# Performance work log

Measured on AMD Instinct MI355X. Metric: run time of the kernel, lower is better.

The kernel has to match this reference:

```python
import jax, jax.numpy as jnp
import numpy as np

N_NODES = 50000
N_HEDGES = 10000
N_MEMB = 800000
IN_SIZE = 256
HEADS = 4
OUT_SIZE = 64


def setup_inputs() -> dict:
    key = jax.random.key(0)
    k1, k2, k3, k4, k5 = jax.random.split(key, 5)
    x = jax.random.normal(k1, (N_NODES, IN_SIZE), dtype=jnp.float32)
    # Linear weight stored as [in, out*heads] so projection is x @ W (same math as torch Linear)
    W = jax.random.normal(k2, (IN_SIZE, OUT_SIZE * HEADS), dtype=jnp.float32) * (1.0 / np.sqrt(IN_SIZE))
    att_e = jax.random.normal(k3, (1, HEADS, OUT_SIZE), dtype=jnp.float32) * 0.1
    node_idx = jax.random.randint(k4, (N_MEMB,), 0, N_NODES, dtype=jnp.int64)
    hedge_idx = jax.random.randint(k5, (N_MEMB,), 0, N_HEDGES, dtype=jnp.int64)
    return {"x": x, "W": W, "att_e": att_e, "node_idx": node_idx,
            "hedge_idx": hedge_idx, "num_hyperedges": N_HEDGES}


def reference(x, W, att_e, node_idx, hedge_idx, num_hyperedges):
    # Dropout is treated as eval-mode identity.
    N = x.shape[0]
    H, D = att_e.shape[1], att_e.shape[2]
    xp = (x @ W).reshape(N, H, D)                                   # [N,H,D]
    # Stage 1: mean-aggregate node features into hyperedges (belongs-to)
    ones = jnp.ones(node_idx.shape[0], dtype=x.dtype)
    deg = jax.ops.segment_sum(ones, hedge_idx, num_segments=num_hyperedges)  # [E]
    he = jax.ops.segment_sum(xp[node_idx], hedge_idx, num_segments=num_hyperedges)
    he = he / jnp.maximum(deg, 1.0)[:, None, None]                  # [E,H,D]
    # Attention logit per hyperedge
    alpha_e = jax.nn.leaky_relu(jnp.sum(he * att_e, axis=-1), 0.2)  # [E,H]
    # Stage 2: edge_softmax over 'contains' edges grouped by destination node
    ae = alpha_e[hedge_idx]                                         # [M,H]
    mx = jax.ops.segment_max(ae, node_idx, num_segments=N)          # [N,H]
    ex = jnp.exp(ae - mx[node_idx])
    den = jax.ops.segment_sum(ex, node_idx, num_segments=N)         # [N,H]
    a = ex / den[node_idx]                                          # [M,H]
    # Attention-weighted scatter-sum of hyperedge features to nodes
    out = jax.ops.segment_sum(he[hedge_idx] * a[:, :, None], node_idx, num_segments=N)  # [N,H,D]
    return out.reshape(N, H * D)
```

## Files before the change

kernel.cpp:

```cpp
#include <hip/hip_runtime.h>
#include <hip/hip_fp16.h>
#include <math.h>

#define N_NODES  50000
#define N_HEDGES 10000
#define N_MEMB   800000
#define KIN      256
#define CH       256
#define HEADS    4
#define HCAP     160
#define NCAP     48
#define GR       16

#define NCHUNK      125
#define CHUNK4      1600
#define XCVT_F4     3200000
#define XCVT_BLOCKS 1563
#define WCVT_BLOCKS 8
#define HED_W       2500
#define NOD_W       12500

typedef _Float16 half2v __attribute__((ext_vector_type(2)));

__device__ inline float2 h2f(unsigned u) {
    __half2 h = __builtin_bit_cast(__half2, u);
    return __half22float2(h);
}
__device__ inline unsigned f2h(float a, float b) {
    return __builtin_bit_cast(unsigned, __floats2half2_rn(a, b));
}
__device__ inline float4 u2tof4(uint2 u) {
    float2 lo = h2f(u.x), hi = h2f(u.y);
    return make_float4(lo.x, lo.y, hi.x, hi.y);
}
__device__ inline void acc4(float4& a, float4 f) {
    a.x += f.x; a.y += f.y; a.z += f.z; a.w += f.w;
}
__device__ inline void fmaU4(float4& A, float4& B, float w, uint4 g) {
    float2 f0 = h2f(g.x), f1 = h2f(g.y), f2 = h2f(g.z), f3 = h2f(g.w);
    A.x += w * f0.x; A.y += w * f0.y; A.z += w * f1.x; A.w += w * f1.y;
    B.x += w * f2.x; B.y += w * f2.y; B.z += w * f3.x; B.w += w * f3.y;
}

__global__ __launch_bounds__(1024)
void k_hist_cvt(const int4* __restrict__ ni4, const int4* __restrict__ hi4,
                unsigned char* __restrict__ htab, unsigned char* __restrict__ ntab,
                const float4* __restrict__ x4, uint2* __restrict__ x16,
                const float* __restrict__ Wf, unsigned* __restrict__ Wp) {
    __shared__ unsigned sh[HED_W + NOD_W];
    int bid = blockIdx.x, tid = threadIdx.x;
    if (bid < NCHUNK) {
        int chunk = bid;
        for (int i = tid; i < HED_W + NOD_W; i += 1024) sh[i] = 0;
        __syncthreads();
        int base4 = chunk * CHUNK4;
        for (int i = tid; i < CHUNK4; i += 1024) {
            int4 e = hi4[base4 + i]; int4 n = ni4[base4 + i];
            #pragma unroll
            for (int k = 0; k < 4; k++) {
                int ev = (&e.x)[k], nv = (&n.x)[k];
                atomicAdd(&sh[ev >> 2], 1u << ((ev & 3) * 8));
                atomicAdd(&sh[HED_W + (nv >> 2)], 1u << ((nv & 3) * 8));
            }
        }
        __syncthreads();
        unsigned* hd = (unsigned*)(htab + (size_t)chunk * N_HEDGES);
        for (int i = tid; i < HED_W; i += 1024) hd[i] = sh[i];
        unsigned* nd = (unsigned*)(ntab + (size_t)chunk * N_NODES);
        for (int i = tid; i < NOD_W; i += 1024) nd[i] = sh[HED_W + i];
    } else if (bid < NCHUNK + XCVT_BLOCKS) {
        int i0 = (bid - NCHUNK) * 2048 + tid;
        #pragma unroll
        for (int r = 0; r < 2; r++) {
            int idx = i0 + r * 1024;
            if (idx < XCVT_F4) {
                float4 v = x4[idx];
                uint2 u; u.x = f2h(v.x, v.y); u.y = f2h(v.z, v.w);
                x16[idx] = u;
            }
        }
    } else {
        int tg = (bid - NCHUNK - XCVT_BLOCKS) * 1024 + tid;
        #pragma unroll
        for (int r = 0; r < 4; r++) {
            int wI = tg + r * 8192;
            int k2 = wI >> 8, c = wI & 255;
            Wp[wI] = f2h(Wf[(size_t)(2 * k2) * CH + c], Wf[(size_t)(2 * k2 + 1) * CH + c]);
        }
    }
}

__global__ __launch_bounds__(1024)
void k_scan(unsigned char* __restrict__ htab, unsigned char* __restrict__ ntab,
            int* __restrict__ hdeg, int* __restrict__ ndeg) {
    int b = blockIdx.x * 1024 + threadIdx.x;
    if (b < N_HEDGES) {
        int run = 0;
        for (int c = 0; c < NCHUNK; c++) {
            size_t idx = (size_t)c * N_HEDGES + b;
            int v = htab[idx];
            htab[idx] = (unsigned char)run;
            run += v;
        }
        hdeg[b] = run;
    } else if (b < N_HEDGES + N_NODES) {
        int nb = b - N_HEDGES;
        int run = 0;
        for (int c = 0; c < NCHUNK; c++) {
            size_t idx = (size_t)c * N_NODES + nb;
            int v = ntab[idx];
            ntab[idx] = (unsigned char)run;
            run += v;
        }
        ndeg[nb] = run;
    }
}

__global__ __launch_bounds__(1024)
void k_place(const int4* __restrict__ ni4, const int4* __restrict__ hi4,
             const unsigned char* __restrict__ htab, const unsigned char* __restrict__ ntab,
             int* __restrict__ hmem, int* __restrict__ nhedge) {
    __shared__ unsigned sh[HED_W + NOD_W];
    int bid = blockIdx.x, tid = threadIdx.x;
    int chunk = bid;
    for (int i = tid; i < HED_W + NOD_W; i += 1024) sh[i] = 0;
    __syncthreads();
    int base4 = chunk * CHUNK4;
    const unsigned char* hoff = htab + (size_t)chunk * N_HEDGES;
    const unsigned char* noff = ntab + (size_t)chunk * N_NODES;
    for (int i = tid; i < CHUNK4; i += 1024) {
        int4 e = hi4[base4 + i]; int4 n = ni4[base4 + i];
        #pragma unroll
        for (int k = 0; k < 4; k++) {
            int ev = (&e.x)[k], nv = (&n.x)[k];
            unsigned oldh = atomicAdd(&sh[ev >> 2], 1u << ((ev & 3) * 8));
            int rh = (int)((oldh >> ((ev & 3) * 8)) & 0xffu);
            int posh = (int)hoff[ev] + rh;
            if (posh < HCAP) hmem[(size_t)ev * HCAP + posh] = nv;
            unsigned oldn = atomicAdd(&sh[HED_W + (nv >> 2)], 1u << ((nv & 3) * 8));
            int rn = (int)((oldn >> ((nv & 3) * 8)) & 0xffu);
            int posn = (int)noff[nv] + rn;
            if (posn < NCAP) nhedge[(size_t)nv * NCAP + posn] = ev;
        }
    }
}

__global__ __launch_bounds__(256, 8)
void k_stage1(const int* __restrict__ hdeg, const int* __restrict__ hmem,
              const uint2* __restrict__ x16, uint2* __restrict__ hx) {
    __shared__ int sidx[4][HCAP];
    int tid = threadIdx.x;
    int w = tid >> 6, lt = tid & 63;
    int e = blockIdx.x * 4 + w;
    int deg = hdeg[e];
    int degC = min(deg, HCAP);
    const int* ml = hmem + (size_t)e * HCAP;
    for (int j = lt; j < degC; j += 64) sidx[w][j] = ml[j];
    __syncthreads();
    float4 ac0 = {0,0,0,0}, ac1 = {0,0,0,0}, ac2 = {0,0,0,0}, ac3 = {0,0,0,0};
    for (int j = 0; j < degC; j += 8) {
        uint2 g[8];
        #pragma unroll
        for (int i = 0; i < 8; i++) {
            int jj = j + i; jj = jj < degC ? jj : degC - 1;
            g[i] = x16[(size_t)sidx[w][jj] * 64 + lt];
        }
        if (j + 0 < degC) acc4(ac0, u2tof4(g[0]));
        if (j + 1 < degC) acc4(ac1, u2tof4(g[1]));
        if (j + 2 < degC) acc4(ac2, u2tof4(g[2]));
        if (j + 3 < degC) acc4(ac3, u2tof4(g[3]));
        if (j + 4 < degC) acc4(ac0, u2tof4(g[4]));
        if (j + 5 < degC) acc4(ac1, u2tof4(g[5]));
        if (j + 6 < degC) acc4(ac2, u2tof4(g[6]));
        if (j + 7 < degC) acc4(ac3, u2tof4(g[7]));
    }
    float sx = (ac0.x + ac1.x) + (ac2.x + ac3.x);
    float sy = (ac0.y + ac1.y) + (ac2.y + ac3.y);
    float sz = (ac0.z + ac1.z) + (ac2.z + ac3.z);
    float sw = (ac0.w + ac1.w) + (ac2.w + ac3.w);
    float inv = deg > 0 ? 1.0f / (float)deg : 0.0f;
    uint2 o; o.x = f2h(sx * inv, sy * inv); o.y = f2h(sz * inv, sw * inv);
    hx[(size_t)e * 64 + lt] = o;
}

__global__ void k_gemm_alpha(const uint2* __restrict__ hx, const unsigned* __restrict__ Wp,
                             const float* __restrict__ att, __half* __restrict__ he,
                             float* __restrict__ alpha) {
    __shared__ unsigned xsp[GR][KIN / 2];
    int tid = threadIdx.x;
    int e0 = blockIdx.x * GR;
    #pragma unroll
    for (int jj = 0; jj < GR * 64 / 256; jj++) {
        int f = jj * 256 + tid;
        int r = f >> 6, k4 = f & 63;
        uint2 u = hx[(size_t)(e0 + r) * 64 + k4];
        xsp[r][k4 * 2] = u.x; xsp[r][k4 * 2 + 1] = u.y;
    }
    __syncthreads();
    float acc[GR];
    #pragma unroll
    for (int r = 0; r < GR; r++) acc[r] = 0.f;
    int c = tid;
    for (int k2 = 0; k2 < KIN / 2; k2++) {
        half2v wv = __builtin_bit_cast(half2v, Wp[k2 * CH + c]);
        #pragma unroll
        for (int r = 0; r < GR; r++) {
            half2v av = __builtin_bit_cast(half2v, xsp[r][k2]);
#if __has_builtin(__builtin_amdgcn_fdot2)
            acc[r] = __builtin_amdgcn_fdot2(av, wv, acc[r], false);
#else
            acc[r] += (float)av.x * (float)wv.x + (float)av.y * (float)wv.y;
#endif
        }
    }
    #pragma unroll
    for (int r = 0; r < GR; r++)
        he[(size_t)(e0 + r) * CH + c] = __float2half_rn(acc[r]);
    float av = att[c];
    int lane = tid & 63, h = tid >> 6;
    #pragma unroll
    for (int r = 0; r < GR; r++) {
        float p = acc[r] * av;
        #pragma unroll
        for (int d = 32; d >= 1; d >>= 1) p += __shfl_xor(p, d, 64);
        if (lane == 0) alpha[(e0 + r) * HEADS + h] = p > 0.f ? p : 0.2f * p;
    }
}

__global__ __launch_bounds__(256, 8)
void k_stage2(const uint4* __restrict__ heu4, const float4* __restrict__ alpha4,
              const int* __restrict__ ndeg, const int* __restrict__ nhedge,
              float4* __restrict__ out) {
    __shared__ int   nh[4][NCAP];
    __shared__ float wl[4][4][NCAP];
    int tid = threadIdx.x;
    int w = tid >> 6, L = tid & 63;
    int half = L >> 5, q = L & 31;
    int n = blockIdx.x * 4 + w;
    int deg = min(ndeg[n], NCAP);
    const int* nl = nhedge + (size_t)n * NCAP;
    if (L < deg) nh[w][L] = nl[L];
    __syncthreads();
    float4 mx = make_float4(-INFINITY, -INFINITY, -INFINITY, -INFINITY);
    float4 w4 = make_float4(0.f, 0.f, 0.f, 0.f);
    float4 aj = mx;
    if (L < deg) { aj = alpha4[nh[w][L]]; mx = aj; }
    #pragma unroll
    for (int d = 32; d >= 1; d >>= 1) {
        mx.x = fmaxf(mx.x, __shfl_xor(mx.x, d, 64));
        mx.y = fmaxf(mx.y, __shfl_xor(mx.y, d, 64));
        mx.z = fmaxf(mx.z, __shfl_xor(mx.z, d, 64));
        mx.w = fmaxf(mx.w, __shfl_xor(mx.w, d, 64));
    }
    if (L < deg) {
        w4.x = __expf(aj.x - mx.x); w4.y = __expf(aj.y - mx.y);
        w4.z = __expf(aj.z - mx.z); w4.w = __expf(aj.w - mx.w);
        wl[w][0][L] = w4.x; wl[w][1][L] = w4.y;
        wl[w][2][L] = w4.z; wl[w][3][L] = w4.w;
    }
    float4 dn = w4;
    #pragma unroll
    for (int d = 32; d >= 1; d >>= 1) {
        dn.x += __shfl_xor(dn.x, d, 64);
        dn.y += __shfl_xor(dn.y, d, 64);
        dn.z += __shfl_xor(dn.z, d, 64);
        dn.w += __shfl_xor(dn.w, d, 64);
    }
    __syncthreads();
    int h = q >> 3;
    float den = h < 2 ? (h == 0 ? dn.x : dn.y) : (h == 2 ? dn.z : dn.w);
    float4 A = make_float4(0.f, 0.f, 0.f, 0.f);
    float4 B = make_float4(0.f, 0.f, 0.f, 0.f);
    if (deg > 0) {
        for (int j = 0; j < deg; j += 8) {
            uint4 g[4]; float wgt[4];
            #pragma unroll
            for (int i = 0; i < 4; i++) {
                int jj = j + 2 * i + half;
                int jc = jj < deg ? jj : deg - 1;
                wgt[i] = jj < deg ? wl[w][h][jc] : 0.f;
                g[i] = heu4[(size_t)nh[w][jc] * 32 + q];
            }
            #pragma unroll
            for (int i = 0; i < 4; i++) fmaU4(A, B, wgt[i], g[i]);
        }
    }
    A.x += __shfl_xor(A.x, 32, 64); A.y += __shfl_xor(A.y, 32, 64);
    A.z += __shfl_xor(A.z, 32, 64); A.w += __shfl_xor(A.w, 32, 64);
    B.x += __shfl_xor(B.x, 32, 64); B.y += __shfl_xor(B.y, 32, 64);
    B.z += __shfl_xor(B.z, 32, 64); B.w += __shfl_xor(B.w, 32, 64);
    if (half == 0) {
        if (deg > 0) {
            float inv = 1.0f / den;
            A.x *= inv; A.y *= inv; A.z *= inv; A.w *= inv;
            B.x *= inv; B.y *= inv; B.z *= inv; B.w *= inv;
        }
        out[(size_t)n * 64 + 2 * q]     = A;
        out[(size_t)n * 64 + 2 * q + 1] = B;
    }
}

extern "C" void kernel_launch(void* const* d_in, const int* in_sizes, int n_in,
                              void* d_out, int out_size, void* d_ws, size_t ws_size,
                              hipStream_t stream) {
    const float* x        = (const float*)d_in[0];
    const float* W        = (const float*)d_in[1];
    const float* att      = (const float*)d_in[2];
    const int*   node_idx = (const int*)d_in[3];
    const int*   hedge_idx= (const int*)d_in[4];
    float4* out4 = (float4*)d_out;

    char* ws = (char*)d_ws;
    size_t o = 0;
    auto alloc = [&](size_t b) { size_t r = o; o += (b + 255) & ~(size_t)255; return r; };
    uint2* hx    = (uint2*)(ws + alloc(sizeof(__half) * (size_t)N_HEDGES * KIN));
    float* alpha = (float*)(ws + alloc(sizeof(float) * (size_t)N_HEDGES * HEADS));
    unsigned* Wp = (unsigned*)(ws + alloc(sizeof(unsigned) * (KIN / 2) * CH));
    int*   hdeg  = (int*)(ws + alloc(sizeof(int) * N_HEDGES));
    int*   ndeg  = (int*)(ws + alloc(sizeof(int) * N_NODES));
    size_t hmem_off = alloc(sizeof(int) * (size_t)N_HEDGES * HCAP);
    int*    hmem = (int*)(ws + hmem_off);
    __half* he   = (__half*)(ws + hmem_off);
    int*   nhedge = (int*)(ws + alloc(sizeof(int) * (size_t)N_NODES * NCAP));
    unsigned char* htab = (unsigned char*)(ws + alloc((size_t)NCHUNK * N_HEDGES));
    unsigned char* ntab = (unsigned char*)(ws + alloc((size_t)NCHUNK * N_NODES));
    if (o > ws_size) return;
    uint2* x16 = (uint2*)d_out;

    k_hist_cvt<<<NCHUNK + XCVT_BLOCKS + WCVT_BLOCKS, 1024, 0, stream>>>(
        (const int4*)node_idx, (const int4*)hedge_idx, htab, ntab,
        (const float4*)x, x16, W, Wp);
    k_scan<<<(N_HEDGES + N_NODES + 1023) / 1024, 1024, 0, stream>>>(htab, ntab, hdeg, ndeg);
    k_place<<<NCHUNK, 1024, 0, stream>>>(
        (const int4*)node_idx, (const int4*)hedge_idx, htab, ntab, hmem, nhedge);
    k_stage1<<<N_HEDGES / 4, 256, 0, stream>>>(hdeg, hmem, x16, hx);
    k_gemm_alpha<<<N_HEDGES / GR, 256, 0, stream>>>(hx, Wp, att, he, alpha);
    k_stage2<<<N_NODES / 4, 256, 0, stream>>>((const uint4*)he, (const float4*)alpha,
                                              ndeg, nhedge, out4);
}
```

Baseline: 193.8 us.

## Fuse hyperedge projection GEMM and attention logit into stage1 kernel

Removes the separate GEMM kernel by having each wave in stage1 project its averaged hyperedge row through W directly and compute the leaky-relu attention logit. This eliminates the intermediate hx buffer round-trip and one launch. In exchange, every wave re-reads the whole packed W matrix instead of amortizing it across 16 rows per block, greatly increasing cache traffic.

```diff
diff --git a/kernel.cpp b/kernel.cpp
--- a/kernel.cpp
+++ b/kernel.cpp
@@ -10,7 +10,6 @@
 #define HEADS    4
 #define HCAP     160
 #define NCAP     48
-#define GR       16
 
 #define NCHUNK      125
 #define CHUNK4      1600
@@ -40,6 +39,13 @@
     float2 f0 = h2f(g.x), f1 = h2f(g.y), f2 = h2f(g.z), f3 = h2f(g.w);
     A.x += w * f0.x; A.y += w * f0.y; A.z += w * f1.x; A.w += w * f1.y;
     B.x += w * f2.x; B.y += w * f2.y; B.z += w * f3.x; B.w += w * f3.y;
+}
+__device__ inline float fdot2w(half2v a, half2v b, float c) {
+#if __has_builtin(__builtin_amdgcn_fdot2)
+    return __builtin_amdgcn_fdot2(a, b, c, false);
+#else
+    return c + (float)a.x * (float)b.x + (float)a.y * (float)b.y;
+#endif
 }
 
 __global__ __launch_bounds__(1024)
@@ -147,8 +153,11 @@
 
 __global__ __launch_bounds__(256, 8)
 void k_stage1(const int* __restrict__ hdeg, const int* __restrict__ hmem,
-              const uint2* __restrict__ x16, uint2* __restrict__ hx) {
+              const uint2* __restrict__ x16, const uint4* __restrict__ Wp4,
+              const float4* __restrict__ att4, uint2* __restrict__ he2,
+              float* __restrict__ alpha) {
     __shared__ int sidx[4][HCAP];
+    __shared__ unsigned hxp[4][KIN / 2];
     int tid = threadIdx.x;
     int w = tid >> 6, lt = tid & 63;
     int e = blockIdx.x * 4 + w;
@@ -179,51 +188,27 @@
     float sz = (ac0.z + ac1.z) + (ac2.z + ac3.z);
     float sw = (ac0.w + ac1.w) + (ac2.w + ac3.w);
     float inv = deg > 0 ? 1.0f / (float)deg : 0.0f;
-    uint2 o; o.x = f2h(sx * inv, sy * inv); o.y = f2h(sz * inv, sw * inv);
-    hx[(size_t)e * 64 + lt] = o;
-}
-
-__global__ void k_gemm_alpha(const uint2* __restrict__ hx, const unsigned* __restrict__ Wp,
-                             const float* __restrict__ att, __half* __restrict__ he,
-                             float* __restrict__ alpha) {
-    __shared__ unsigned xsp[GR][KIN / 2];
-    int tid = threadIdx.x;
-    int e0 = blockIdx.x * GR;
-    #pragma unroll
-    for (int jj = 0; jj < GR * 64 / 256; jj++) {
-        int f = jj * 256 + tid;
-        int r = f >> 6, k4 = f & 63;
-        uint2 u = hx[(size_t)(e0 + r) * 64 + k4];
-        xsp[r][k4 * 2] = u.x; xsp[r][k4 * 2 + 1] = u.y;
-    }
-    __syncthreads();
-    float acc[GR];
-    #pragma unroll
-    for (int r = 0; r < GR; r++) acc[r] = 0.f;
-    int c = tid;
+    hxp[w][2 * lt]     = f2h(sx * inv, sy * inv);
+    hxp[w][2 * lt + 1] = f2h(sz * inv, sw * inv);
+    __syncthreads();
+    float a0 = 0.f, a1 = 0.f, a2 = 0.f, a3 = 0.f;
     for (int k2 = 0; k2 < KIN / 2; k2++) {
-        half2v wv = __builtin_bit_cast(half2v, Wp[k2 * CH + c]);
-        #pragma unroll
-        for (int r = 0; r < GR; r++) {
-            half2v av = __builtin_bit_cast(half2v, xsp[r][k2]);
-#if __has_builtin(__builtin_amdgcn_fdot2)
-            acc[r] = __builtin_amdgcn_fdot2(av, wv, acc[r], false);
-#else
-            acc[r] += (float)av.x * (float)wv.x + (float)av.y * (float)wv.y;
-#endif
-        }
-    }
-    #pragma unroll
-    for (int r = 0; r < GR; r++)
-        he[(size_t)(e0 + r) * CH + c] = __float2half_rn(acc[r]);
-    float av = att[c];
-    int lane = tid & 63, h = tid >> 6;
-    #pragma unroll
-    for (int r = 0; r < GR; r++) {
-        float p = acc[r] * av;
-        #pragma unroll
-        for (int d = 32; d >= 1; d >>= 1) p += __shfl_xor(p, d, 64);
-        if (lane == 0) alpha[(e0 + r) * HEADS + h] = p > 0.f ? p : 0.2f * p;
+        half2v hv = __builtin_bit_cast(half2v, hxp[w][k2]);
+        uint4 wq = Wp4[(size_t)k2 * 64 + lt];
+        a0 = fdot2w(hv, __builtin_bit_cast(half2v, wq.x), a0);
+        a1 = fdot2w(hv, __builtin_bit_cast(half2v, wq.y), a1);
+        a2 = fdot2w(hv, __builtin_bit_cast(half2v, wq.z), a2);
+        a3 = fdot2w(hv, __builtin_bit_cast(half2v, wq.w), a3);
+    }
+    uint2 o; o.x = f2h(a0, a1); o.y = f2h(a2, a3);
+    he2[(size_t)e * 64 + lt] = o;
+    float4 a4 = att4[lt];
+    float p = a0 * a4.x + a1 * a4.y + a2 * a4.z + a3 * a4.w;
+    p += __shfl_xor(p, 1, 64); p += __shfl_xor(p, 2, 64);
+    p += __shfl_xor(p, 4, 64); p += __shfl_xor(p, 8, 64);
+    if ((lt & 15) == 0) {
+        int h = lt >> 4;
+        alpha[e * HEADS + h] = p > 0.f ? p : 0.2f * p;
     }
 }
 
@@ -313,14 +298,12 @@
     char* ws = (char*)d_ws;
     size_t o = 0;
     auto alloc = [&](size_t b) { size_t r = o; o += (b + 255) & ~(size_t)255; return r; };
-    uint2* hx    = (uint2*)(ws + alloc(sizeof(__half) * (size_t)N_HEDGES * KIN));
     float* alpha = (float*)(ws + alloc(sizeof(float) * (size_t)N_HEDGES * HEADS));
     unsigned* Wp = (unsigned*)(ws + alloc(sizeof(unsigned) * (KIN / 2) * CH));
     int*   hdeg  = (int*)(ws + alloc(sizeof(int) * N_HEDGES));
     int*   ndeg  = (int*)(ws + alloc(sizeof(int) * N_NODES));
-    size_t hmem_off = alloc(sizeof(int) * (size_t)N_HEDGES * HCAP);
-    int*    hmem = (int*)(ws + hmem_off);
-    __half* he   = (__half*)(ws + hmem_off);
+    int*   hmem  = (int*)(ws + alloc(sizeof(int) * (size_t)N_HEDGES * HCAP));
+    uint2* he2   = (uint2*)(ws + alloc(sizeof(__half) * (size_t)N_HEDGES * CH));
     int*   nhedge = (int*)(ws + alloc(sizeof(int) * (size_t)N_NODES * NCAP));
     unsigned char* htab = (unsigned char*)(ws + alloc((size_t)NCHUNK * N_HEDGES));
     unsigned char* ntab = (unsigned char*)(ws + alloc((size_t)NCHUNK * N_NODES));
@@ -333,8 +316,8 @@
     k_scan<<<(N_HEDGES + N_NODES + 1023) / 1024, 1024, 0, stream>>>(htab, ntab, hdeg, ndeg);
     k_place<<<NCHUNK, 1024, 0, stream>>>(
         (const int4*)node_idx, (const int4*)hedge_idx, htab, ntab, hmem, nhedge);
-    k_stage1<<<N_HEDGES / 4, 256, 0, stream>>>(hdeg, hmem, x16, hx);
-    k_gemm_alpha<<<N_HEDGES / GR, 256, 0, stream>>>(hx, Wp, att, he, alpha);
-    k_stage2<<<N_NODES / 4, 256, 0, stream>>>((const uint4*)he, (const float4*)alpha,
+    k_stage1<<<N_HEDGES / 4, 256, 0, stream>>>(hdeg, hmem, x16, (const uint4*)Wp,
+                                               (const float4*)att, he2, alpha);
+    k_stage2<<<N_NODES / 4, 256, 0, stream>>>((const uint4*)he2, (const float4*)alpha,
                                               ndeg, nhedge, out4);
 }
```

Result: faster. 189.6 us (-2.2%).
